# Kernel tuning notes

Measured on AMD Instinct MI355X. Metric: run time of the kernel, lower is better.

The kernel has to match this reference:

```python
import jax, jax.numpy as jnp
import numpy as np

B, S, D = 16, 16, 4096          # batch, q_len, model dim
H, KVH = 32, 8                  # query heads, kv heads (GQA)
HD = D // H                     # head_dim = 128
N_REP = H // KVH                # 4
MAX_B, MAX_S = 16, 4096         # cache dims
ROPE_BASE = 10000.0


def apply_rope(x, start_pos):
    # x: (b, s, h, d); rotate consecutive pairs (x[2i], x[2i+1]) like view_as_complex
    b, s, h, d = x.shape
    theta = 1.0 / (ROPE_BASE ** (jnp.arange(0, d, 2, dtype=jnp.float32) / d))  # (d/2,)
    pos = jnp.arange(start_pos, start_pos + s, dtype=jnp.float32)              # (s,)
    f = pos[:, None] * theta[None, :]                                          # (s, d/2)
    cos = jnp.cos(f)[None, :, None, :]
    sin = jnp.sin(f)[None, :, None, :]
    xp = x.astype(jnp.float32).reshape(b, s, h, d // 2, 2)
    xr, xi = xp[..., 0], xp[..., 1]
    out = jnp.stack([xr * cos - xi * sin, xr * sin + xi * cos], axis=-1)
    return out.reshape(b, s, h, d).astype(x.dtype)


def setup_inputs() -> dict:
    key = jax.random.key(0)
    ks = jax.random.split(key, 8)
    w = 0.02
    return {
        "x": jax.random.normal(ks[0], (B, S, D), jnp.float32),
        "Wq": jax.random.normal(ks[1], (D, H * HD), jnp.float32) * w,
        "Wk": jax.random.normal(ks[2], (D, KVH * HD), jnp.float32) * w,
        "Wv": jax.random.normal(ks[3], (D, KVH * HD), jnp.float32) * w,
        "Wo": jax.random.normal(ks[4], (H * HD, D), jnp.float32) * w,
        # caches hold (simulated) past context keys/values
        "cache_k": jax.random.normal(ks[5], (MAX_B, MAX_S, KVH, HD), jnp.float32),
        "cache_v": jax.random.normal(ks[6], (MAX_B, MAX_S, KVH, HD), jnp.float32),
        "start_pos": MAX_S - S,  # 4080
    }


def reference(x, Wq, Wk, Wv, Wo, cache_k, cache_v, start_pos):
    b, s, _ = x.shape
    kv_len = start_pos + s

    xq = (x @ Wq).reshape(b, s, H, HD)
    xk = (x @ Wk).reshape(b, s, KVH, HD)
    xv = (x @ Wv).reshape(b, s, KVH, HD)

    xq = apply_rope(xq, start_pos)
    xk = apply_rope(xk, start_pos)

    # KV-cache append
    cache_k = cache_k.at[:b, start_pos:start_pos + s].set(xk)
    cache_v = cache_v.at[:b, start_pos:start_pos + s].set(xv)
    keys = cache_k[:b, :kv_len]    # (b, t, kvh, d)
    values = cache_v[:b, :kv_len]  # (b, t, kvh, d)

    # GQA: group query heads per kv head instead of materializing the repeat.
    # repeat_heads maps kv head k -> query heads [k*n_rep, (k+1)*n_rep).
    q = xq.transpose(0, 2, 1, 3).reshape(b, KVH, N_REP, s, HD)

    scores = jnp.einsum('bkrsd,btkd->bkrst', q, keys) / np.sqrt(HD).astype(np.float32)
    attn = jax.nn.softmax(scores.astype(jnp.float32), axis=-1).astype(q.dtype)
    ctx = jnp.einsum('bkrst,btkd->bkrsd', attn, values)  # (b, kvh, n_rep, s, d)

    ctx = ctx.reshape(b, H, s, HD).transpose(0, 2, 1, 3).reshape(b, s, H * HD)
    return ctx @ Wo
```

## Files before the change

kernel.cpp:

```cpp
#include <hip/hip_runtime.h>
#include <hip/hip_bf16.h>

#define D_    4096
#define KVH_  8
#define HD_   128
#define MAXS_ 4096
#define M_    256
#define NCH   8
#define TPC   (MAXS_ / NCH)

using frag_ab = __attribute__((ext_vector_type(8))) short;
using frag_cd = __attribute__((ext_vector_type(4))) float;

__device__ __forceinline__ short bfb(float f) {
  union { float f; unsigned u; } cv; cv.f = f;
  unsigned u = cv.u;
  return (short)((u + 0x7fffu + ((u >> 16) & 1u)) >> 16);
}

__global__ __launch_bounds__(256) void prep_kernel(
    const float* __restrict__ Wq, const float* __restrict__ Wk,
    const float* __restrict__ Wv, const float* __restrict__ Wo,
    const float* __restrict__ x,
    short* __restrict__ Wqkv_t,
    short* __restrict__ Wo_t,
    short* __restrict__ x_bf)
{
  int idx = blockIdx.x;
  int tid = threadIdx.x;
  if (idx >= 10240) {
    int j0 = (idx - 10240) * 256 + tid;
    const float4* xs = (const float4*)x;
    for (int j = j0; j < (M_ * D_) / 4; j += 16 * 256) {
      float4 v = xs[j];
      short4 o; o.x = bfb(v.x); o.y = bfb(v.y); o.z = bfb(v.z); o.w = bfb(v.w);
      *(short4*)(x_bf + (size_t)j * 4) = o;
    }
    return;
  }
  const float* W; short* Wt; int N; int tile;
  if (idx < 4096)      { W = Wq; Wt = Wqkv_t;                          N = 4096; tile = idx; }
  else if (idx < 5120) { W = Wk; Wt = Wqkv_t + (size_t)4096 * 4096;    N = 1024; tile = idx - 4096; }
  else if (idx < 6144) { W = Wv; Wt = Wqkv_t + (size_t)5120 * 4096;    N = 1024; tile = idx - 5120; }
  else                 { W = Wo; Wt = Wo_t;                            N = 4096; tile = idx - 6144; }
  int ntn = N >> 6;
  int tk = tile / ntn, tn = tile - tk * ntn;
  int k0 = tk << 6, n0 = tn << 6;
  __shared__ short tb[64 * 66];
#pragma unroll
  for (int p = 0; p < 4; p++) {
    int seg = p * 256 + tid;
    int r = seg >> 4, c4 = (seg & 15) << 2;
    float4 v = *(const float4*)(W + (size_t)(k0 + r) * N + n0 + c4);
    tb[(c4 + 0) * 66 + r] = bfb(v.x);
    tb[(c4 + 1) * 66 + r] = bfb(v.y);
    tb[(c4 + 2) * 66 + r] = bfb(v.z);
    tb[(c4 + 3) * 66 + r] = bfb(v.w);
  }
  __syncthreads();
#pragma unroll
  for (int p = 0; p < 4; p++) {
    int seg = p * 256 + tid;
    int n = seg >> 4, c4 = (seg & 15) << 2;
    short4 o;
    o.x = tb[n * 66 + c4 + 0];
    o.y = tb[n * 66 + c4 + 1];
    o.z = tb[n * 66 + c4 + 2];
    o.w = tb[n * 66 + c4 + 3];
    *(short4*)(Wt + (size_t)(n0 + n) * 4096 + k0 + c4) = o;
  }
}

#define LDT 72

template<int MODE>
__global__ __launch_bounds__(256) void gemm_bf(
    const short* __restrict__ A, const short* __restrict__ Bt,
    short* __restrict__ q_bf, short* __restrict__ k_bf, short* __restrict__ v_bf,
    float* __restrict__ Cf, const int* __restrict__ sp)
{
  __shared__ __align__(16) short lds_a[64 * LDT];
  __shared__ __align__(16) short lds_b[64 * LDT];
  int tid = threadIdx.x;
  int wave = tid >> 6, lane = tid & 63, quad = lane >> 4, l16 = lane & 15;
  int m0 = blockIdx.y * 64;
  int n0 = blockIdx.x * 64;

  const frag_cd fz = {0.f, 0.f, 0.f, 0.f};
  frag_cd acc[4];
#pragma unroll
  for (int i = 0; i < 4; i++) acc[i] = fz;

  for (int kk = 0; kk < 4096; kk += 64) {
    __syncthreads();
#pragma unroll
    for (int p = 0; p < 2; p++) {
      int seg = p * 256 + tid;
      int m = seg >> 3, k8 = (seg & 7) << 3;
      *(frag_ab*)(&lds_a[m * LDT + k8]) = *(const frag_ab*)(A + (size_t)(m0 + m) * 4096 + kk + k8);
      *(frag_ab*)(&lds_b[m * LDT + k8]) = *(const frag_ab*)(Bt + (size_t)(n0 + m) * 4096 + kk + k8);
    }
    __syncthreads();
#pragma unroll
    for (int k0 = 0; k0 < 64; k0 += 32) {
      frag_ab af = *(const frag_ab*)(&lds_a[(wave * 16 + l16) * LDT + k0 + quad * 8]);
#pragma unroll
      for (int nt = 0; nt < 4; nt++) {
        frag_ab bf = *(const frag_ab*)(&lds_b[(nt * 16 + l16) * LDT + k0 + quad * 8]);
        acc[nt] = __builtin_amdgcn_mfma_f32_16x16x32_bf16(af, bf, acc[nt], 0, 0, 0);
      }
    }
  }

  int start_pos = (MODE == 0) ? *sp : 0;
#pragma unroll
  for (int nt = 0; nt < 4; nt++) {
    int n = n0 + nt * 16 + l16;
#pragma unroll
    for (int r = 0; r < 4; r++) {
      int m = m0 + wave * 16 + quad * 4 + r;
      float v = acc[nt][r];
      if (MODE == 1) {
        Cf[(size_t)m * 4096 + n] = v;
      } else {
        float outv = v;
        if (n < 5120) {
          float partner = __shfl_xor(v, 1);
          int hd = n & (HD_ - 1);
          float theta = exp2f(-(float)(hd >> 1) * 0.2076205059304601f);
          float fr = (float)(start_pos + (m & 15)) * theta;
          float sn, cs;
          sincosf(fr, &sn, &cs);
          outv = v * cs + ((n & 1) ? partner * sn : -partner * sn);
        }
        short ob = bfb(outv);
        if (n < 4096)      q_bf[(size_t)m * 4096 + n] = ob;
        else if (n < 5120) k_bf[(size_t)m * 1024 + n - 4096] = ob;
        else               v_bf[(size_t)m * 1024 + n - 5120] = ob;
      }
    }
  }
}

#define KLD 136
#define VLD 72
#define PLD 72

__global__ __launch_bounds__(256, 4) void attn_kernel(
    const short* __restrict__ qb,
    const short* __restrict__ kb,
    const short* __restrict__ vb,
    const float* __restrict__ cache_k,
    const float* __restrict__ cache_v,
    float* __restrict__ part_ctx,
    float* __restrict__ part_m,
    float* __restrict__ part_l,
    const int* __restrict__ sp)
{
  __shared__ __align__(16) short k_s[64 * KLD];
  __shared__ __align__(16) short vT[HD_ * VLD];
  short* p_s = k_s;

  int chunk = blockIdx.x, kvh = blockIdx.y, b = blockIdx.z;
  int tid = threadIdx.x;
  int wave = tid >> 6, lane = tid & 63, quad = lane >> 4, l16 = lane & 15;
  int start_pos = *sp;

  frag_ab qf[4];
  {
    const short* qrow = qb + (size_t)(b * 16 + l16) * D_ + (kvh * 4 + wave) * HD_;
#pragma unroll
    for (int k0 = 0; k0 < 4; k0++)
      qf[k0] = *(const frag_ab*)(qrow + k0 * 32 + quad * 8);
  }

  const frag_cd fz = {0.f, 0.f, 0.f, 0.f};
  frag_cd acc_o[8];
#pragma unroll
  for (int i = 0; i < 8; i++) acc_o[i] = fz;
  float m_i[4], l_i[4];
#pragma unroll
  for (int r = 0; r < 4; r++) { m_i[r] = -1e30f; l_i[r] = 0.f; }

  int rloc = tid >> 5;
  int lane32 = tid & 31;
  int hd4 = lane32 * 4;
  const float scale = 0.08838834764831845f;

  for (int it = 0; it < TPC / 64; it++) {
    int t0 = chunk * TPC + it * 64;
    __syncthreads();
#pragma unroll
    for (int pass = 0; pass < 8; pass++) {
      int row = pass * 8 + rloc;
      int t = t0 + row;
      short4 kq, vq;
      if (t < start_pos) {
        size_t off = (((size_t)b * MAXS_ + t) * KVH_ + kvh) * HD_ + hd4;
        float4 k4 = *(const float4*)(cache_k + off);
        float4 v4 = *(const float4*)(cache_v + off);
        kq.x = bfb(k4.x); kq.y = bfb(k4.y); kq.z = bfb(k4.z); kq.w = bfb(k4.w);
        vq.x = bfb(v4.x); vq.y = bfb(v4.y); vq.z = bfb(v4.z); vq.w = bfb(v4.w);
      } else {
        int s = t - start_pos;
        size_t off = (size_t)(b * 16 + s) * (KVH_ * HD_) + kvh * HD_ + hd4;
        kq = *(const short4*)(kb + off);
        vq = *(const short4*)(vb + off);
      }
      *(short4*)(&k_s[row * KLD + hd4]) = kq;
      int cb = row >> 3, wi = row & 7;
      {
        int hd = hd4 + 0; vT[hd * VLD + (((cb ^ ((hd >> 3) & 7)) << 3) | wi)] = kq.x = vq.x, vq.x;
      }
      vT[(hd4 + 0) * VLD + (((cb ^ (((hd4 + 0) >> 3) & 7)) << 3) | wi)] = vq.x;
      vT[(hd4 + 1) * VLD + (((cb ^ (((hd4 + 1) >> 3) & 7)) << 3) | wi)] = vq.y;
      vT[(hd4 + 2) * VLD + (((cb ^ (((hd4 + 2) >> 3) & 7)) << 3) | wi)] = vq.z;
      vT[(hd4 + 3) * VLD + (((cb ^ (((hd4 + 3) >> 3) & 7)) << 3) | wi)] = vq.w;
    }
    __syncthreads();

    frag_cd sc[4];
#pragma unroll
    for (int i = 0; i < 4; i++) sc[i] = fz;
#pragma unroll
    for (int k0 = 0; k0 < HD_; k0 += 32) {
#pragma unroll
      for (int nt = 0; nt < 4; nt++) {
        frag_ab bfm = *(const frag_ab*)(&k_s[(nt * 16 + l16) * KLD + k0 + quad * 8]);
        sc[nt] = __builtin_amdgcn_mfma_f32_16x16x32_bf16(qf[k0 >> 5], bfm, sc[nt], 0, 0, 0);
      }
    }

    float alpha[4];
#pragma unroll
    for (int r = 0; r < 4; r++) {
      float mx = fmaxf(fmaxf(sc[0][r], sc[1][r]), fmaxf(sc[2][r], sc[3][r])) * scale;
#pragma unroll
      for (int off = 1; off < 16; off <<= 1) mx = fmaxf(mx, __shfl_xor(mx, off));
      float mnew = fmaxf(m_i[r], mx);
      alpha[r] = __expf(m_i[r] - mnew);
      m_i[r] = mnew;
      float rsum = 0.f;
#pragma unroll
      for (int nt = 0; nt < 4; nt++) {
        float p = __expf(sc[nt][r] * scale - mnew);
        sc[nt][r] = p;
        rsum += p;
      }
#pragma unroll
      for (int off = 1; off < 16; off <<= 1) rsum += __shfl_xor(rsum, off);
      l_i[r] = l_i[r] * alpha[r] + rsum;
    }
#pragma unroll
    for (int nt = 0; nt < 8; nt++)
#pragma unroll
      for (int r = 0; r < 4; r++) acc_o[nt][r] *= alpha[r];

    __syncthreads();
#pragma unroll
    for (int r = 0; r < 4; r++)
#pragma unroll
      for (int nt = 0; nt < 4; nt++)
        p_s[(wave * 16 + quad * 4 + r) * PLD + nt * 16 + l16] = bfb(sc[nt][r]);

#pragma unroll
    for (int k0 = 0; k0 < 64; k0 += 32) {
      frag_ab af = *(const frag_ab*)(&p_s[(wave * 16 + l16) * PLD + k0 + quad * 8]);
      int tb = (k0 >> 3) + quad;
#pragma unroll
      for (int nt = 0; nt < 8; nt++) {
        int hd = nt * 16 + l16;
        frag_ab bfm = *(const frag_ab*)(&vT[hd * VLD + ((tb ^ ((hd >> 3) & 7)) << 3)]);
        acc_o[nt] = __builtin_amdgcn_mfma_f32_16x16x32_bf16(af, bfm, acc_o[nt], 0, 0, 0);
      }
    }
  }

  int blk = ((b * 8 + kvh) << 3) + chunk;
#pragma unroll
  for (int nt = 0; nt < 8; nt++)
#pragma unroll
    for (int r = 0; r < 4; r++) {
      int qrow = wave * 16 + quad * 4 + r;
      part_ctx[((size_t)blk * 64 + qrow) * HD_ + nt * 16 + l16] = acc_o[nt][r];
    }
  if (l16 == 0) {
#pragma unroll
    for (int r = 0; r < 4; r++) {
      int qrow = wave * 16 + quad * 4 + r;
      part_m[blk * 64 + qrow] = m_i[r];
      part_l[blk * 64 + qrow] = l_i[r];
    }
  }
}

__global__ __launch_bounds__(256) void combine_kernel(
    const float* __restrict__ part_ctx, const float* __restrict__ part_m,
    const float* __restrict__ part_l, short* __restrict__ ctx_bf)
{
  int bk = blockIdx.x;
  int b = bk >> 3, kvh = bk & 7;
  int tid = threadIdx.x;
  __shared__ float w_s[8][64];
  __shared__ float inv_l[64];
  if (tid < 64) {
    float M = -1e30f;
#pragma unroll
    for (int c = 0; c < 8; c++) M = fmaxf(M, part_m[(bk * 8 + c) * 64 + tid]);
    float ls = 0.f;
#pragma unroll
    for (int c = 0; c < 8; c++) {
      float w = __expf(part_m[(bk * 8 + c) * 64 + tid] - M);
      w_s[c][tid] = w;
      ls += part_l[(bk * 8 + c) * 64 + tid] * w;
    }
    inv_l[tid] = 1.f / ls;
  }
  __syncthreads();
  for (int idx = tid; idx < 64 * 128; idx += 256) {
    int qrow = idx >> 7, hd = idx & 127;
    float acc = 0.f;
#pragma unroll
    for (int c = 0; c < 8; c++)
      acc += part_ctx[((size_t)(bk * 8 + c) * 64 + qrow) * HD_ + hd] * w_s[c][qrow];
    float val = acc * inv_l[qrow];
    int r = qrow >> 4, s = qrow & 15;
    ctx_bf[(size_t)(b * 16 + s) * D_ + (kvh * 4 + r) * HD_ + hd] = bfb(val);
  }
}

extern "C" void kernel_launch(void* const* d_in, const int* in_sizes, int n_in,
                              void* d_out, int out_size, void* d_ws, size_t ws_size,
                              hipStream_t stream)
{
  const float* x       = (const float*)d_in[0];
  const float* Wq      = (const float*)d_in[1];
  const float* Wk      = (const float*)d_in[2];
  const float* Wv      = (const float*)d_in[3];
  const float* Wo      = (const float*)d_in[4];
  const float* cache_k = (const float*)d_in[5];
  const float* cache_v = (const float*)d_in[6];
  const int*   sp      = (const int*)d_in[7];

  char* w = (char*)d_ws;
  auto alloc = [&](size_t bytes) { char* p = w; w += (bytes + 255) & ~(size_t)255; return p; };
  short* Wqkv_t = (short*)alloc((size_t)6144 * 4096 * 2);
  short* Wo_t   = (short*)alloc((size_t)4096 * 4096 * 2);
  short* x_bf   = (short*)alloc((size_t)M_ * 4096 * 2);
  short* q_bf   = (short*)alloc((size_t)M_ * 4096 * 2);
  short* k_bf   = (short*)alloc((size_t)M_ * 1024 * 2);
  short* v_bf   = (short*)alloc((size_t)M_ * 1024 * 2);
  short* ctx_bf = (short*)alloc((size_t)M_ * 4096 * 2);
  float* part_ctx = (float*)alloc((size_t)1024 * 64 * 128 * 4);
  float* part_m   = (float*)alloc((size_t)1024 * 64 * 4);
  float* part_l   = (float*)alloc((size_t)1024 * 64 * 4);

  prep_kernel<<<10256, 256, 0, stream>>>(Wq, Wk, Wv, Wo, x, Wqkv_t, Wo_t, x_bf);

  gemm_bf<0><<<dim3(6144 / 64, M_ / 64), 256, 0, stream>>>(
      x_bf, Wqkv_t, q_bf, k_bf, v_bf, nullptr, sp);

  attn_kernel<<<dim3(NCH, 8, 16), 256, 0, stream>>>(
      q_bf, k_bf, v_bf, cache_k, cache_v, part_ctx, part_m, part_l, sp);

  combine_kernel<<<128, 256, 0, stream>>>(part_ctx, part_m, part_l, ctx_bf);

  gemm_bf<1><<<dim3(4096 / 64, M_ / 64), 256, 0, stream>>>(
      ctx_bf, Wo_t, nullptr, nullptr, nullptr, (float*)d_out, sp);
}
```

Measured before the change: 891.8 us.

## Split-K 128x128 GEMMs with async LDS loads, separate RoPE pass, prefetch KV in attention

The GEMMs become 128x128-tile, split-K=8 kernels that fill LDS with global_load_lds and reduce partial sums into pre-zeroed fp32 buffers with atomics. RoPE and the bf16 conversion move out of the QKV GEMM epilogue into a separate elementwise kernel. The attention kernel register-prefetches the next K/V tile while the current one is processed, and its occupancy hint drops to 3. The weight transpose now writes 16-byte vectors. These changes target the low parallelism and data reuse of the 64x64 GEMMs and the exposed load latency in attention, at the cost of atomic traffic, extra zeroing and conversion kernels, and nondeterministic summation order.

New measurement: 1.020 ms. +14.3%, slower.

```diff
diff --git a/kernel.cpp b/kernel.cpp
--- a/kernel.cpp
+++ b/kernel.cpp
@@ -17,6 +17,28 @@
   unsigned u = cv.u;
   return (short)((u + 0x7fffu + ((u >> 16) & 1u)) >> 16);
 }
+__device__ __forceinline__ float b2f(short s) {
+  union { float f; unsigned u; } cv; cv.u = ((unsigned)(unsigned short)s) << 16; return cv.f;
+}
+__device__ __forceinline__ short4 cvt4(float4 v) {
+  short4 o; o.x = bfb(v.x); o.y = bfb(v.y); o.z = bfb(v.z); o.w = bfb(v.w); return o;
+}
+__device__ __forceinline__ float4 f4_of_s4(short4 s) {
+  return make_float4(b2f(s.x), b2f(s.y), b2f(s.z), b2f(s.w));
+}
+
+typedef const unsigned int __attribute__((address_space(1)))* gas_t;
+typedef unsigned int __attribute__((address_space(3)))* las_t;
+__device__ __forceinline__ void gl_lds16(const void* g, void* l) {
+  __builtin_amdgcn_global_load_lds((gas_t)(unsigned long long)g,
+                                   (las_t)(unsigned)(unsigned long long)l, 16, 0, 0);
+}
+
+__global__ __launch_bounds__(256) void zero_kernel(float4* __restrict__ p, int n4) {
+  int i = blockIdx.x * 256 + threadIdx.x;
+  int st = gridDim.x * 256;
+  for (; i < n4; i += st) p[i] = make_float4(0.f, 0.f, 0.f, 0.f);
+}
 
 __global__ __launch_bounds__(256) void prep_kernel(
     const float* __restrict__ Wq, const float* __restrict__ Wk,
@@ -32,9 +54,7 @@
     int j0 = (idx - 10240) * 256 + tid;
     const float4* xs = (const float4*)x;
     for (int j = j0; j < (M_ * D_) / 4; j += 16 * 256) {
-      float4 v = xs[j];
-      short4 o; o.x = bfb(v.x); o.y = bfb(v.y); o.z = bfb(v.z); o.w = bfb(v.w);
-      *(short4*)(x_bf + (size_t)j * 4) = o;
+      *(short4*)(x_bf + (size_t)j * 4) = cvt4(xs[j]);
     }
     return;
   }
@@ -46,116 +66,122 @@
   int ntn = N >> 6;
   int tk = tile / ntn, tn = tile - tk * ntn;
   int k0 = tk << 6, n0 = tn << 6;
-  __shared__ short tb[64 * 66];
+  __shared__ __align__(16) short tb[64 * 72];
 #pragma unroll
   for (int p = 0; p < 4; p++) {
     int seg = p * 256 + tid;
     int r = seg >> 4, c4 = (seg & 15) << 2;
     float4 v = *(const float4*)(W + (size_t)(k0 + r) * N + n0 + c4);
-    tb[(c4 + 0) * 66 + r] = bfb(v.x);
-    tb[(c4 + 1) * 66 + r] = bfb(v.y);
-    tb[(c4 + 2) * 66 + r] = bfb(v.z);
-    tb[(c4 + 3) * 66 + r] = bfb(v.w);
+    tb[(c4 + 0) * 72 + r] = bfb(v.x);
+    tb[(c4 + 1) * 72 + r] = bfb(v.y);
+    tb[(c4 + 2) * 72 + r] = bfb(v.z);
+    tb[(c4 + 3) * 72 + r] = bfb(v.w);
   }
   __syncthreads();
 #pragma unroll
-  for (int p = 0; p < 4; p++) {
+  for (int p = 0; p < 2; p++) {
     int seg = p * 256 + tid;
-    int n = seg >> 4, c4 = (seg & 15) << 2;
-    short4 o;
-    o.x = tb[n * 66 + c4 + 0];
-    o.y = tb[n * 66 + c4 + 1];
-    o.z = tb[n * 66 + c4 + 2];
-    o.w = tb[n * 66 + c4 + 3];
-    *(short4*)(Wt + (size_t)(n0 + n) * 4096 + k0 + c4) = o;
-  }
-}
-
-#define LDT 72
-
-template<int MODE>
-__global__ __launch_bounds__(256) void gemm_bf(
+    int n = seg >> 3, k8 = (seg & 7) << 3;
+    frag_ab v = *(const frag_ab*)(&tb[n * 72 + k8]);
+    *(frag_ab*)(Wt + (size_t)(n0 + n) * 4096 + k0 + k8) = v;
+  }
+}
+
+__global__ __launch_bounds__(256, 3) void gemm_sk(
     const short* __restrict__ A, const short* __restrict__ Bt,
-    short* __restrict__ q_bf, short* __restrict__ k_bf, short* __restrict__ v_bf,
-    float* __restrict__ Cf, const int* __restrict__ sp)
-{
-  __shared__ __align__(16) short lds_a[64 * LDT];
-  __shared__ __align__(16) short lds_b[64 * LDT];
+    float* __restrict__ out, int Nout)
+{
+  __shared__ __align__(16) short lds_a[128 * 64];
+  __shared__ __align__(16) short lds_b[128 * 64];
   int tid = threadIdx.x;
   int wave = tid >> 6, lane = tid & 63, quad = lane >> 4, l16 = lane & 15;
-  int m0 = blockIdx.y * 64;
-  int n0 = blockIdx.x * 64;
+  int n0 = blockIdx.x * 128, m0 = blockIdx.y * 128;
+  int lrow = lane >> 3, lcol = lane & 7;
+  int mq = (wave >> 1) * 64, nq = (wave & 1) * 64;
 
   const frag_cd fz = {0.f, 0.f, 0.f, 0.f};
-  frag_cd acc[4];
-#pragma unroll
-  for (int i = 0; i < 4; i++) acc[i] = fz;
-
-  for (int kk = 0; kk < 4096; kk += 64) {
+  frag_cd acc[4][4];
+#pragma unroll
+  for (int i = 0; i < 4; i++)
+#pragma unroll
+    for (int j = 0; j < 4; j++) acc[i][j] = fz;
+
+  int kbeg = blockIdx.z * 512;
+  for (int kk = kbeg; kk < kbeg + 512; kk += 64) {
     __syncthreads();
 #pragma unroll
-    for (int p = 0; p < 2; p++) {
-      int seg = p * 256 + tid;
-      int m = seg >> 3, k8 = (seg & 7) << 3;
-      *(frag_ab*)(&lds_a[m * LDT + k8]) = *(const frag_ab*)(A + (size_t)(m0 + m) * 4096 + kk + k8);
-      *(frag_ab*)(&lds_b[m * LDT + k8]) = *(const frag_ab*)(Bt + (size_t)(n0 + m) * 4096 + kk + k8);
+    for (int i = 0; i < 4; i++) {
+      int r = wave * 32 + i * 8;
+      gl_lds16(A  + (size_t)(m0 + r + lrow) * 4096 + kk + lcol * 8, &lds_a[r * 64]);
+      gl_lds16(Bt + (size_t)(n0 + r + lrow) * 4096 + kk + lcol * 8, &lds_b[r * 64]);
     }
     __syncthreads();
 #pragma unroll
     for (int k0 = 0; k0 < 64; k0 += 32) {
-      frag_ab af = *(const frag_ab*)(&lds_a[(wave * 16 + l16) * LDT + k0 + quad * 8]);
-#pragma unroll
-      for (int nt = 0; nt < 4; nt++) {
-        frag_ab bf = *(const frag_ab*)(&lds_b[(nt * 16 + l16) * LDT + k0 + quad * 8]);
-        acc[nt] = __builtin_amdgcn_mfma_f32_16x16x32_bf16(af, bf, acc[nt], 0, 0, 0);
+      frag_ab af[4], bf[4];
+#pragma unroll
+      for (int i = 0; i < 4; i++) {
+        af[i] = *(const frag_ab*)(&lds_a[(mq + i * 16 + l16) * 64 + k0 + quad * 8]);
+        bf[i] = *(const frag_ab*)(&lds_b[(nq + i * 16 + l16) * 64 + k0 + quad * 8]);
       }
-    }
-  }
-
-  int start_pos = (MODE == 0) ? *sp : 0;
-#pragma unroll
-  for (int nt = 0; nt < 4; nt++) {
-    int n = n0 + nt * 16 + l16;
-#pragma unroll
-    for (int r = 0; r < 4; r++) {
-      int m = m0 + wave * 16 + quad * 4 + r;
-      float v = acc[nt][r];
-      if (MODE == 1) {
-        Cf[(size_t)m * 4096 + n] = v;
-      } else {
-        float outv = v;
-        if (n < 5120) {
-          float partner = __shfl_xor(v, 1);
-          int hd = n & (HD_ - 1);
-          float theta = exp2f(-(float)(hd >> 1) * 0.2076205059304601f);
-          float fr = (float)(start_pos + (m & 15)) * theta;
-          float sn, cs;
-          sincosf(fr, &sn, &cs);
-          outv = v * cs + ((n & 1) ? partner * sn : -partner * sn);
-        }
-        short ob = bfb(outv);
-        if (n < 4096)      q_bf[(size_t)m * 4096 + n] = ob;
-        else if (n < 5120) k_bf[(size_t)m * 1024 + n - 4096] = ob;
-        else               v_bf[(size_t)m * 1024 + n - 5120] = ob;
+#pragma unroll
+      for (int mi = 0; mi < 4; mi++)
+#pragma unroll
+        for (int ni = 0; ni < 4; ni++)
+          acc[mi][ni] = __builtin_amdgcn_mfma_f32_16x16x32_bf16(af[mi], bf[ni], acc[mi][ni], 0, 0, 0);
+    }
+  }
+#pragma unroll
+  for (int mi = 0; mi < 4; mi++)
+#pragma unroll
+    for (int ni = 0; ni < 4; ni++)
+#pragma unroll
+      for (int r = 0; r < 4; r++) {
+        int m = m0 + mq + mi * 16 + quad * 4 + r;
+        int n = n0 + nq + ni * 16 + l16;
+        atomicAdd(&out[(size_t)m * Nout + n], acc[mi][ni][r]);
       }
-    }
-  }
+}
+
+__global__ __launch_bounds__(256) void rope_convert(
+    const float* __restrict__ qkv, short* __restrict__ q_bf,
+    short* __restrict__ k_bf, short* __restrict__ v_bf, const int* __restrict__ sp)
+{
+  int start_pos = *sp;
+  int i = blockIdx.x * 256 + threadIdx.x;
+  int m = i / 1536;
+  int n = (i - m * 1536) * 4;
+  float4 x = *(const float4*)(qkv + (size_t)m * 6144 + n);
+  short4 o;
+  if (n < 5120) {
+    int pi = (n & 127) >> 1;
+    float pos = (float)(start_pos + (m & 15));
+    const float C = 0.2076205059304601f;
+    float t0 = exp2f(-(float)pi * C);
+    float t1 = exp2f(-(float)(pi + 1) * C);
+    float s0, c0, s1, c1;
+    sincosf(pos * t0, &s0, &c0);
+    sincosf(pos * t1, &s1, &c1);
+    o.x = bfb(x.x * c0 - x.y * s0); o.y = bfb(x.x * s0 + x.y * c0);
+    o.z = bfb(x.z * c1 - x.w * s1); o.w = bfb(x.z * s1 + x.w * c1);
+  } else {
+    o = cvt4(x);
+  }
+  if (n < 4096)      *(short4*)(q_bf + (size_t)m * 4096 + n) = o;
+  else if (n < 5120) *(short4*)(k_bf + (size_t)m * 1024 + (n - 4096)) = o;
+  else               *(short4*)(v_bf + (size_t)m * 1024 + (n - 5120)) = o;
 }
 
 #define KLD 136
 #define VLD 72
 #define PLD 72
 
-__global__ __launch_bounds__(256, 4) void attn_kernel(
-    const short* __restrict__ qb,
-    const short* __restrict__ kb,
+__global__ __launch_bounds__(256, 3) void attn_kernel(
+    const short* __restrict__ qb, const short* __restrict__ kb,
     const short* __restrict__ vb,
-    const float* __restrict__ cache_k,
-    const float* __restrict__ cache_v,
-    float* __restrict__ part_ctx,
-    float* __restrict__ part_m,
-    float* __restrict__ part_l,
-    const int* __restrict__ sp)
+    const float* __restrict__ cache_k, const float* __restrict__ cache_v,
+    float* __restrict__ part_ctx, float* __restrict__ part_m,
+    float* __restrict__ part_l, const int* __restrict__ sp)
 {
   __shared__ __align__(16) short k_s[64 * KLD];
   __shared__ __align__(16) short vT[HD_ * VLD];
@@ -165,6 +191,9 @@
   int tid = threadIdx.x;
   int wave = tid >> 6, lane = tid & 63, quad = lane >> 4, l16 = lane & 15;
   int start_pos = *sp;
+  int rloc = tid >> 5;
+  int hd4 = (tid & 31) * 4;
+  const float scale = 0.08838834764831845f;
 
   frag_ab qf[4];
   {
@@ -182,40 +211,42 @@
 #pragma unroll
   for (int r = 0; r < 4; r++) { m_i[r] = -1e30f; l_i[r] = 0.f; }
 
-  int rloc = tid >> 5;
-  int lane32 = tid & 31;
-  int hd4 = lane32 * 4;
-  const float scale = 0.08838834764831845f;
+  auto ld_pair = [&](int t, float4& kq, float4& vq) {
+    if (t < start_pos) {
+      size_t off = (((size_t)b * MAXS_ + t) * KVH_ + kvh) * HD_ + hd4;
+      kq = *(const float4*)(cache_k + off);
+      vq = *(const float4*)(cache_v + off);
+    } else {
+      int s = t - start_pos;
+      size_t off = (size_t)(b * 16 + s) * (KVH_ * HD_) + kvh * HD_ + hd4;
+      kq = f4_of_s4(*(const short4*)(kb + off));
+      vq = f4_of_s4(*(const short4*)(vb + off));
+    }
+  };
+
+  float4 kr[8], vr[8];
+#pragma unroll
+  for (int p = 0; p < 8; p++) ld_pair(chunk * TPC + p * 8 + rloc, kr[p], vr[p]);
 
   for (int it = 0; it < TPC / 64; it++) {
-    int t0 = chunk * TPC + it * 64;
+    short4 kc16[8], vc16[8];
+#pragma unroll
+    for (int p = 0; p < 8; p++) { kc16[p] = cvt4(kr[p]); vc16[p] = cvt4(vr[p]); }
+    if (it + 1 < TPC / 64) {
+      int tn = chunk * TPC + (it + 1) * 64;
+#pragma unroll
+      for (int p = 0; p < 8; p++) ld_pair(tn + p * 8 + rloc, kr[p], vr[p]);
+    }
     __syncthreads();
 #pragma unroll
-    for (int pass = 0; pass < 8; pass++) {
-      int row = pass * 8 + rloc;
-      int t = t0 + row;
-      short4 kq, vq;
-      if (t < start_pos) {
-        size_t off = (((size_t)b * MAXS_ + t) * KVH_ + kvh) * HD_ + hd4;
-        float4 k4 = *(const float4*)(cache_k + off);
-        float4 v4 = *(const float4*)(cache_v + off);
-        kq.x = bfb(k4.x); kq.y = bfb(k4.y); kq.z = bfb(k4.z); kq.w = bfb(k4.w);
-        vq.x = bfb(v4.x); vq.y = bfb(v4.y); vq.z = bfb(v4.z); vq.w = bfb(v4.w);
-      } else {
-        int s = t - start_pos;
-        size_t off = (size_t)(b * 16 + s) * (KVH_ * HD_) + kvh * HD_ + hd4;
-        kq = *(const short4*)(kb + off);
-        vq = *(const short4*)(vb + off);
-      }
-      *(short4*)(&k_s[row * KLD + hd4]) = kq;
+    for (int p = 0; p < 8; p++) {
+      int row = p * 8 + rloc;
+      *(short4*)(&k_s[row * KLD + hd4]) = kc16[p];
       int cb = row >> 3, wi = row & 7;
-      {
-        int hd = hd4 + 0; vT[hd * VLD + (((cb ^ ((hd >> 3) & 7)) << 3) | wi)] = kq.x = vq.x, vq.x;
-      }
-      vT[(hd4 + 0) * VLD + (((cb ^ (((hd4 + 0) >> 3) & 7)) << 3) | wi)] = vq.x;
-      vT[(hd4 + 1) * VLD + (((cb ^ (((hd4 + 1) >> 3) & 7)) << 3) | wi)] = vq.y;
-      vT[(hd4 + 2) * VLD + (((cb ^ (((hd4 + 2) >> 3) & 7)) << 3) | wi)] = vq.z;
-      vT[(hd4 + 3) * VLD + (((cb ^ (((hd4 + 3) >> 3) & 7)) << 3) | wi)] = vq.w;
+      vT[(hd4 + 0) * VLD + (((cb ^ (((hd4 + 0) >> 3) & 7)) << 3) | wi)] = vc16[p].x;
+      vT[(hd4 + 1) * VLD + (((cb ^ (((hd4 + 1) >> 3) & 7)) << 3) | wi)] = vc16[p].y;
+      vT[(hd4 + 2) * VLD + (((cb ^ (((hd4 + 2) >> 3) & 7)) << 3) | wi)] = vc16[p].z;
+      vT[(hd4 + 3) * VLD + (((cb ^ (((hd4 + 3) >> 3) & 7)) << 3) | wi)] = vc16[p].w;
     }
     __syncthreads();
 
@@ -266,11 +297,11 @@
 #pragma unroll
     for (int k0 = 0; k0 < 64; k0 += 32) {
       frag_ab af = *(const frag_ab*)(&p_s[(wave * 16 + l16) * PLD + k0 + quad * 8]);
-      int tb = (k0 >> 3) + quad;
+      int tbk = (k0 >> 3) + quad;
 #pragma unroll
       for (int nt = 0; nt < 8; nt++) {
         int hd = nt * 16 + l16;
-        frag_ab bfm = *(const frag_ab*)(&vT[hd * VLD + ((tb ^ ((hd >> 3) & 7)) << 3)]);
+        frag_ab bfm = *(const frag_ab*)(&vT[hd * VLD + ((tbk ^ ((hd >> 3) & 7)) << 3)]);
         acc_o[nt] = __builtin_amdgcn_mfma_f32_16x16x32_bf16(af, bfm, acc_o[nt], 0, 0, 0);
       }
     }
@@ -344,27 +375,28 @@
 
   char* w = (char*)d_ws;
   auto alloc = [&](size_t bytes) { char* p = w; w += (bytes + 255) & ~(size_t)255; return p; };
-  short* Wqkv_t = (short*)alloc((size_t)6144 * 4096 * 2);
-  short* Wo_t   = (short*)alloc((size_t)4096 * 4096 * 2);
-  short* x_bf   = (short*)alloc((size_t)M_ * 4096 * 2);
-  short* q_bf   = (short*)alloc((size_t)M_ * 4096 * 2);
-  short* k_bf   = (short*)alloc((size_t)M_ * 1024 * 2);
-  short* v_bf   = (short*)alloc((size_t)M_ * 1024 * 2);
-  short* ctx_bf = (short*)alloc((size_t)M_ * 4096 * 2);
+  short* Wqkv_t  = (short*)alloc((size_t)6144 * 4096 * 2);
+  short* Wo_t    = (short*)alloc((size_t)4096 * 4096 * 2);
+  short* x_bf    = (short*)alloc((size_t)M_ * 4096 * 2);
+  float* qkv_acc = (float*)alloc((size_t)M_ * 6144 * 4);
+  short* q_bf    = (short*)alloc((size_t)M_ * 4096 * 2);
+  short* k_bf    = (short*)alloc((size_t)M_ * 1024 * 2);
+  short* v_bf    = (short*)alloc((size_t)M_ * 1024 * 2);
+  short* ctx_bf  = (short*)alloc((size_t)M_ * 4096 * 2);
   float* part_ctx = (float*)alloc((size_t)1024 * 64 * 128 * 4);
   float* part_m   = (float*)alloc((size_t)1024 * 64 * 4);
   float* part_l   = (float*)alloc((size_t)1024 * 64 * 4);
 
   prep_kernel<<<10256, 256, 0, stream>>>(Wq, Wk, Wv, Wo, x, Wqkv_t, Wo_t, x_bf);
-
-  gemm_bf<0><<<dim3(6144 / 64, M_ / 64), 256, 0, stream>>>(
-      x_bf, Wqkv_t, q_bf, k_bf, v_bf, nullptr, sp);
+  zero_kernel<<<1536, 256, 0, stream>>>((float4*)qkv_acc, (M_ * 6144) / 4);
+  zero_kernel<<<1024, 256, 0, stream>>>((float4*)d_out, (M_ * 4096) / 4);
+
+  gemm_sk<<<dim3(48, 2, 8), 256, 0, stream>>>(x_bf, Wqkv_t, qkv_acc, 6144);
+  rope_convert<<<1536, 256, 0, stream>>>(qkv_acc, q_bf, k_bf, v_bf, sp);
 
   attn_kernel<<<dim3(NCH, 8, 16), 256, 0, stream>>>(
       q_bf, k_bf, v_bf, cache_k, cache_v, part_ctx, part_m, part_l, sp);
-
   combine_kernel<<<128, 256, 0, stream>>>(part_ctx, part_m, part_l, ctx_bf);
 
-  gemm_bf<1><<<dim3(4096 / 64, M_ / 64), 256, 0, stream>>>(
-      ctx_bf, Wo_t, nullptr, nullptr, nullptr, (float*)d_out, sp);
-}
+  gemm_sk<<<dim3(32, 2, 8), 256, 0, stream>>>(ctx_bf, Wo_t, (float*)d_out, 4096);
+}
```
